# Performance work log

Measured on AMD Instinct MI355X. Metric: run time of the kernel, lower is better.

## Reference

```python
import jax, jax.numpy as jnp
import numpy as np

B = 128          # batch of predictions
C = 1024         # number of constraints
N = 512          # number of atoms appearing in constraints (minimal subset)
NUM_CLASSES = 1024
BODY_P = 0.02    # body sparsity


def setup_inputs() -> dict:
    rng = np.random.default_rng(0)
    # distinct sorted atom indices into the full class space
    atoms = np.sort(rng.permutation(NUM_CLASSES)[:N]).astype(np.int64)
    # each constraint has one head literal: one-hot in pos_head OR neg_head
    head_atom = rng.integers(0, N, size=C)
    head_sign = rng.random(C) < 0.5
    pos_head = np.zeros((C, N), np.float32)
    neg_head = np.zeros((C, N), np.float32)
    rows = np.arange(C)
    pos_head[rows[head_sign], head_atom[head_sign]] = 1.0
    neg_head[rows[~head_sign], head_atom[~head_sign]] = 1.0
    # sparse disjoint 0/1 body masks, head atom excluded from its own body
    pos_body = (rng.random((C, N)) < BODY_P).astype(np.float32)
    neg_body = ((rng.random((C, N)) < BODY_P) & (pos_body == 0)).astype(np.float32)
    pos_body[rows, head_atom] = 0.0
    neg_body[rows, head_atom] = 0.0
    key = jax.random.key(0)
    preds = jax.random.uniform(key, (B, NUM_CLASSES), dtype=jnp.float32)  # probs in [0,1]
    return {
        "preds": preds,
        "pos_head": jnp.asarray(pos_head),
        "neg_head": jnp.asarray(neg_head),
        "pos_body": jnp.asarray(pos_body),
        "neg_body": jnp.asarray(neg_body),
        "atoms": jnp.asarray(atoms),
    }


def reference(preds, pos_head, neg_head, pos_body, neg_body, atoms):
    # to_minimal: gather atom subset  [B, N]
    m = preds[:, atoms]
    # body_rev[b,c,j] = pos_body + m*(neg_body - pos_body)
    #   = (1-m) where body literal positive, m where negative, 0 otherwise
    body_rev = pos_body[None] + m[:, None, :] * (neg_body - pos_body)[None]  # [B,C,N]
    # candidate body satisfaction degree per constraint
    body_min = 1.0 - jnp.max(body_rev, axis=2)  # [B,C]
    # scatter candidates to head atoms via one-hot head masks (max-reduce over cons)
    lb = jnp.max(body_min[:, :, None] * pos_head[None], axis=1)        # [B,N]
    ub = 1.0 - jnp.max(body_min[:, :, None] * neg_head[None], axis=1)  # [B,N]
    lo = jnp.minimum(lb, ub)
    hi = jnp.maximum(lb, ub)
    updated = jnp.maximum(lo, jnp.minimum(hi, m))
    # from_minimal: scatter updated atoms back into full prediction vector
    return preds.at[:, atoms].set(updated)
```

## Files before the change

### kernel.cpp

```cpp
#include <hip/hip_runtime.h>

#define Bsz 128
#define Csz 1024
#define Nsz 512
#define NCsz 1024
#define CAP 64
#define MCAP 32
#define NT2 512

__global__ __launch_bounds__(256) void k_scan(
    const float* __restrict__ preds,
    const float* __restrict__ pos_head, const float* __restrict__ neg_head,
    const float* __restrict__ pos_body, const float* __restrict__ neg_body,
    const int* __restrict__ atoms,
    float* __restrict__ mT,
    int* __restrict__ pos_list, int* __restrict__ neg_list,
    int* __restrict__ pos_cnt, int* __restrict__ neg_cnt,
    int* __restrict__ head_of)
{
    int blk = blockIdx.x, tid = threadIdx.x;
    if (blk < 256) {
        int b   = tid & (Bsz - 1);
        int col = 2 * blk + (tid >> 7);
        mT[col * Bsz + b] = preds[b * NCsz + atoms[col]];
    } else {
        __shared__ int cnts[4][2];
        int wave = tid >> 6, lane = tid & 63;
        int c = (blk - 256) * 4 + wave;
        if (lane == 0) { cnts[wave][0] = 0; cnts[wave][1] = 0; }
        const float4* pb4 = (const float4*)(pos_body + c * Nsz);
        const float4* nb4 = (const float4*)(neg_body + c * Nsz);
        const float4* ph4 = (const float4*)(pos_head + c * Nsz);
        const float4* nh4 = (const float4*)(neg_head + c * Nsz);
        for (int k = 0; k < 2; k++) {
            int q = k * 64 + lane;
            float4 p  = pb4[q];
            float4 nb = nb4[q];
            float4 ph = ph4[q];
            float4 nh = nh4[q];
            int n0 = q * 4;
            if (p.x  != 0.f) { int s = atomicAdd(&cnts[wave][0], 1); if (s < CAP) pos_list[c * CAP + s] = n0;     }
            if (p.y  != 0.f) { int s = atomicAdd(&cnts[wave][0], 1); if (s < CAP) pos_list[c * CAP + s] = n0 + 1; }
            if (p.z  != 0.f) { int s = atomicAdd(&cnts[wave][0], 1); if (s < CAP) pos_list[c * CAP + s] = n0 + 2; }
            if (p.w  != 0.f) { int s = atomicAdd(&cnts[wave][0], 1); if (s < CAP) pos_list[c * CAP + s] = n0 + 3; }
            if (nb.x != 0.f) { int s = atomicAdd(&cnts[wave][1], 1); if (s < CAP) neg_list[c * CAP + s] = n0;     }
            if (nb.y != 0.f) { int s = atomicAdd(&cnts[wave][1], 1); if (s < CAP) neg_list[c * CAP + s] = n0 + 1; }
            if (nb.z != 0.f) { int s = atomicAdd(&cnts[wave][1], 1); if (s < CAP) neg_list[c * CAP + s] = n0 + 2; }
            if (nb.w != 0.f) { int s = atomicAdd(&cnts[wave][1], 1); if (s < CAP) neg_list[c * CAP + s] = n0 + 3; }
            if (ph.x != 0.f) head_of[c] = ((n0    ) << 1) | 1;
            if (ph.y != 0.f) head_of[c] = ((n0 + 1) << 1) | 1;
            if (ph.z != 0.f) head_of[c] = ((n0 + 2) << 1) | 1;
            if (ph.w != 0.f) head_of[c] = ((n0 + 3) << 1) | 1;
            if (nh.x != 0.f) head_of[c] = ((n0    ) << 1);
            if (nh.y != 0.f) head_of[c] = ((n0 + 1) << 1);
            if (nh.z != 0.f) head_of[c] = ((n0 + 2) << 1);
            if (nh.w != 0.f) head_of[c] = ((n0 + 3) << 1);
        }
        if (lane == 0) {
            pos_cnt[c] = min(cnts[wave][0], CAP);
            neg_cnt[c] = min(cnts[wave][1], CAP);
        }
    }
}

__global__ __launch_bounds__(NT2) void k_apply(
    const float* __restrict__ preds,
    const float* __restrict__ mT,
    const int* __restrict__ pos_list, const int* __restrict__ neg_list,
    const int* __restrict__ pos_cnt, const int* __restrict__ neg_cnt,
    const int* __restrict__ head_of,
    const int* __restrict__ atoms,
    float* __restrict__ out)
{
    int blk = blockIdx.x, tid = threadIdx.x;
    if (blk < Nsz) {
        __shared__ int   matched[MCAP];
        __shared__ int   mcnt;
        __shared__ float lbs[4][Bsz];
        __shared__ float ubs[4][Bsz];
        const int n = blk;
        if (tid == 0) mcnt = 0;
        __syncthreads();
        for (int i = tid; i < Csz; i += NT2) {
            int h = head_of[i];
            if ((h >> 1) == n) {
                int s = atomicAdd(&mcnt, 1);
                if (s < MCAP) matched[s] = (i << 1) | (h & 1);
            }
        }
        __syncthreads();
        int q = tid >> 7, b = tid & (Bsz - 1);
        float lb = 0.f, ubm = 0.f;
        int mc = min(mcnt, MCAP);
        for (int k = q; k < mc; k += 4) {
            int c    = matched[k] >> 1;
            int sign = matched[k] & 1;
            const int* pl = pos_list + c * CAP;
            const int* nl = neg_list + c * CAP;
            int pc = pos_cnt[c], nc = neg_cnt[c];
            float acc = 0.f;
            for (int e = 0; e < pc; e++) acc = fmaxf(acc, 1.f - mT[pl[e] * Bsz + b]);
            for (int e = 0; e < nc; e++) acc = fmaxf(acc, mT[nl[e] * Bsz + b]);
            float bm = 1.f - acc;
            if (sign) lb = fmaxf(lb, bm); else ubm = fmaxf(ubm, bm);
        }
        lbs[q][b] = lb; ubs[q][b] = ubm;
        __syncthreads();
        if (q == 0) {
            lb  = fmaxf(fmaxf(lbs[0][b], lbs[1][b]), fmaxf(lbs[2][b], lbs[3][b]));
            ubm = fmaxf(fmaxf(ubs[0][b], ubs[1][b]), fmaxf(ubs[2][b], ubs[3][b]));
            float ub = 1.f - ubm;
            float m  = mT[n * Bsz + b];
            float lo = fminf(lb, ub), hi = fmaxf(lb, ub);
            out[b * NCsz + atoms[n]] = fmaxf(lo, fminf(hi, m));
        }
    } else {
        __shared__ char isatom[NCsz];
        int p = blk - Nsz;
        for (int i = tid; i < NCsz; i += NT2) isatom[i] = 0;
        __syncthreads();
        isatom[atoms[tid]] = 1;
        __syncthreads();
        for (int k = 0; k < 4; k++) {
            int t = p * (4 * NT2) + k * NT2 + tid;
            int b = t >> 10, j = t & (NCsz - 1);
            if (!isatom[j]) out[b * NCsz + j] = preds[b * NCsz + j];
        }
    }
}

extern "C" void kernel_launch(void* const* d_in, const int* in_sizes, int n_in,
                              void* d_out, int out_size, void* d_ws, size_t ws_size,
                              hipStream_t stream)
{
    const float* preds    = (const float*)d_in[0];
    const float* pos_head = (const float*)d_in[1];
    const float* neg_head = (const float*)d_in[2];
    const float* pos_body = (const float*)d_in[3];
    const float* neg_body = (const float*)d_in[4];
    const int*   atoms    = (const int*)d_in[5];
    float* out = (float*)d_out;

    char* ws = (char*)d_ws;
    float* mT       = (float*)(ws);
    int*   pos_list = (int*)(ws + 65536u * 4);
    int*   neg_list = (int*)(ws + 131072u * 4);
    int*   pos_cnt  = (int*)(ws + 196608u * 4);
    int*   neg_cnt  = pos_cnt + Csz;
    int*   head_of  = neg_cnt + Csz;

    k_scan<<<512, 256, 0, stream>>>(preds, pos_head, neg_head, pos_body, neg_body, atoms,
                                    mT, pos_list, neg_list, pos_cnt, neg_cnt, head_of);

    k_apply<<<576, NT2, 0, stream>>>(preds, mT, pos_list, neg_list, pos_cnt, neg_cnt,
                                     head_of, atoms, out);
}
```

Measured before the change: 84.21 us.

## Parallelize per-constraint body eval with atomicMax scatter into bound buffers

Replaces the per-atom gather kernel, which scanned all constraints to find matching heads and then evaluated them serially, with a per-constraint kernel that evaluates each body once and scatters its result to the head atom using atomicMax on float bits. A third kernel combines the lower and upper bounds with the clamp and writes the atom columns. The full preds copy moves into the first kernel as a float4 copy that is later overwritten at atom columns, and the bound buffers are zeroed there too. This removes the per-block scan over all head_of entries and the load imbalance between atoms, at the cost of an extra kernel launch and global atomics. Using atomicMax on unsigned bits relies on the values being non-negative.

```diff
diff --git a/kernel.cpp b/kernel.cpp
--- a/kernel.cpp
+++ b/kernel.cpp
@@ -5,28 +5,29 @@
 #define Nsz 512
 #define NCsz 1024
 #define CAP 64
-#define MCAP 32
-#define NT2 512
 
-__global__ __launch_bounds__(256) void k_scan(
+__global__ __launch_bounds__(256) void k_pre(
     const float* __restrict__ preds,
     const float* __restrict__ pos_head, const float* __restrict__ neg_head,
     const float* __restrict__ pos_body, const float* __restrict__ neg_body,
     const int* __restrict__ atoms,
-    float* __restrict__ mT,
+    float* __restrict__ mT, unsigned* __restrict__ bounds,
     int* __restrict__ pos_list, int* __restrict__ neg_list,
     int* __restrict__ pos_cnt, int* __restrict__ neg_cnt,
-    int* __restrict__ head_of)
+    int* __restrict__ head_of,
+    float* __restrict__ out)
 {
     int blk = blockIdx.x, tid = threadIdx.x;
-    if (blk < 256) {
+    if (blk < 128) {
+        ((uint4*)bounds)[blk * 256 + tid] = make_uint4(0u, 0u, 0u, 0u);
+    } else if (blk < 384) {
         int b   = tid & (Bsz - 1);
-        int col = 2 * blk + (tid >> 7);
+        int col = 2 * (blk - 128) + (tid >> 7);
         mT[col * Bsz + b] = preds[b * NCsz + atoms[col]];
-    } else {
+    } else if (blk < 640) {
         __shared__ int cnts[4][2];
         int wave = tid >> 6, lane = tid & 63;
-        int c = (blk - 256) * 4 + wave;
+        int c = (blk - 384) * 4 + wave;
         if (lane == 0) { cnts[wave][0] = 0; cnts[wave][1] = 0; }
         const float4* pb4 = (const float4*)(pos_body + c * Nsz);
         const float4* nb4 = (const float4*)(neg_body + c * Nsz);
@@ -60,73 +61,56 @@
             pos_cnt[c] = min(cnts[wave][0], CAP);
             neg_cnt[c] = min(cnts[wave][1], CAP);
         }
+    } else {
+        int q = (blk - 640) * 256 + tid;
+        ((float4*)out)[q] = ((const float4*)preds)[q];
     }
 }
 
-__global__ __launch_bounds__(NT2) void k_apply(
-    const float* __restrict__ preds,
+__global__ __launch_bounds__(256) void k_body(
     const float* __restrict__ mT,
     const int* __restrict__ pos_list, const int* __restrict__ neg_list,
     const int* __restrict__ pos_cnt, const int* __restrict__ neg_cnt,
     const int* __restrict__ head_of,
-    const int* __restrict__ atoms,
-    float* __restrict__ out)
+    unsigned* __restrict__ bounds)
 {
-    int blk = blockIdx.x, tid = threadIdx.x;
-    if (blk < Nsz) {
-        __shared__ int   matched[MCAP];
-        __shared__ int   mcnt;
-        __shared__ float lbs[4][Bsz];
-        __shared__ float ubs[4][Bsz];
-        const int n = blk;
-        if (tid == 0) mcnt = 0;
-        __syncthreads();
-        for (int i = tid; i < Csz; i += NT2) {
-            int h = head_of[i];
-            if ((h >> 1) == n) {
-                int s = atomicAdd(&mcnt, 1);
-                if (s < MCAP) matched[s] = (i << 1) | (h & 1);
-            }
-        }
-        __syncthreads();
-        int q = tid >> 7, b = tid & (Bsz - 1);
-        float lb = 0.f, ubm = 0.f;
-        int mc = min(mcnt, MCAP);
-        for (int k = q; k < mc; k += 4) {
-            int c    = matched[k] >> 1;
-            int sign = matched[k] & 1;
-            const int* pl = pos_list + c * CAP;
-            const int* nl = neg_list + c * CAP;
-            int pc = pos_cnt[c], nc = neg_cnt[c];
-            float acc = 0.f;
-            for (int e = 0; e < pc; e++) acc = fmaxf(acc, 1.f - mT[pl[e] * Bsz + b]);
-            for (int e = 0; e < nc; e++) acc = fmaxf(acc, mT[nl[e] * Bsz + b]);
-            float bm = 1.f - acc;
-            if (sign) lb = fmaxf(lb, bm); else ubm = fmaxf(ubm, bm);
-        }
-        lbs[q][b] = lb; ubs[q][b] = ubm;
-        __syncthreads();
-        if (q == 0) {
-            lb  = fmaxf(fmaxf(lbs[0][b], lbs[1][b]), fmaxf(lbs[2][b], lbs[3][b]));
-            ubm = fmaxf(fmaxf(ubs[0][b], ubs[1][b]), fmaxf(ubs[2][b], ubs[3][b]));
-            float ub = 1.f - ubm;
-            float m  = mT[n * Bsz + b];
-            float lo = fminf(lb, ub), hi = fmaxf(lb, ub);
-            out[b * NCsz + atoms[n]] = fmaxf(lo, fminf(hi, m));
-        }
-    } else {
-        __shared__ char isatom[NCsz];
-        int p = blk - Nsz;
-        for (int i = tid; i < NCsz; i += NT2) isatom[i] = 0;
-        __syncthreads();
-        isatom[atoms[tid]] = 1;
-        __syncthreads();
-        for (int k = 0; k < 4; k++) {
-            int t = p * (4 * NT2) + k * NT2 + tid;
-            int b = t >> 10, j = t & (NCsz - 1);
-            if (!isatom[j]) out[b * NCsz + j] = preds[b * NCsz + j];
-        }
-    }
+    __shared__ int sp[2][CAP];
+    __shared__ int sn[2][CAP];
+    int tid = threadIdx.x;
+    int cl = tid >> 7, r = tid & 127;
+    int c = blockIdx.x * 2 + cl;
+    if (r < CAP) sp[cl][r]       = pos_list[c * CAP + r];
+    else         sn[cl][r - CAP] = neg_list[c * CAP + (r - CAP)];
+    __syncthreads();
+
+    int b  = tid & (Bsz - 1);
+    int pc = pos_cnt[c], nc = neg_cnt[c];
+    float acc = 0.f;
+    #pragma unroll 4
+    for (int e = 0; e < pc; e++) acc = fmaxf(acc, 1.f - mT[sp[cl][e] * Bsz + b]);
+    #pragma unroll 4
+    for (int e = 0; e < nc; e++) acc = fmaxf(acc, mT[sn[cl][e] * Bsz + b]);
+
+    int h = head_of[c];
+    unsigned* lbmax = bounds;
+    unsigned* ubmax = bounds + Bsz * Nsz;
+    unsigned* dst = (h & 1) ? lbmax : ubmax;
+    atomicMax(dst + (h >> 1) * Bsz + b, __float_as_uint(1.f - acc));
+}
+
+__global__ __launch_bounds__(256) void k_final(
+    const float* __restrict__ mT,
+    const unsigned* __restrict__ bounds,
+    const int* __restrict__ atoms, float* __restrict__ out)
+{
+    int t = blockIdx.x * 256 + threadIdx.x;
+    int b = t & (Bsz - 1), n = t >> 7;
+    int i = n * Bsz + b;
+    float m  = mT[i];
+    float lb = __uint_as_float(bounds[i]);
+    float ub = 1.f - __uint_as_float(bounds[Bsz * Nsz + i]);
+    float lo = fminf(lb, ub), hi = fmaxf(lb, ub);
+    out[b * NCsz + atoms[n]] = fmaxf(lo, fminf(hi, m));
 }
 
 extern "C" void kernel_launch(void* const* d_in, const int* in_sizes, int n_in,
@@ -142,16 +126,20 @@
     float* out = (float*)d_out;
 
     char* ws = (char*)d_ws;
-    float* mT       = (float*)(ws);
-    int*   pos_list = (int*)(ws + 65536u * 4);
-    int*   neg_list = (int*)(ws + 131072u * 4);
-    int*   pos_cnt  = (int*)(ws + 196608u * 4);
-    int*   neg_cnt  = pos_cnt + Csz;
-    int*   head_of  = neg_cnt + Csz;
+    float*    mT       = (float*)(ws);
+    unsigned* bounds   = (unsigned*)(ws + 65536u * 4);
+    int*      pos_list = (int*)(ws + 196608u * 4);
+    int*      neg_list = (int*)(ws + 262144u * 4);
+    int*      pos_cnt  = (int*)(ws + 327680u * 4);
+    int*      neg_cnt  = pos_cnt + Csz;
+    int*      head_of  = neg_cnt + Csz;
 
-    k_scan<<<512, 256, 0, stream>>>(preds, pos_head, neg_head, pos_body, neg_body, atoms,
-                                    mT, pos_list, neg_list, pos_cnt, neg_cnt, head_of);
+    k_pre<<<768, 256, 0, stream>>>(preds, pos_head, neg_head, pos_body, neg_body, atoms,
+                                   mT, bounds, pos_list, neg_list,
+                                   pos_cnt, neg_cnt, head_of, out);
 
-    k_apply<<<576, NT2, 0, stream>>>(preds, mT, pos_list, neg_list, pos_cnt, neg_cnt,
-                                     head_of, atoms, out);
+    k_body<<<Csz / 2, 256, 0, stream>>>(mT, pos_list, neg_list, pos_cnt, neg_cnt,
+                                        head_of, bounds);
+
+    k_final<<<256, 256, 0, stream>>>(mT, bounds, atoms, out);
 }
```

Result: faster. 77.12 us (-8.4%).
